# Performance work log

Hardware: AMD Instinct MI355X
Metric: run time of the kernel (lower is better)

## Reference

```python
import jax, jax.numpy as jnp
import numpy as np

HEADS = 16
HEAD_DIM = 64

def setup_inputs() -> dict:
    key = jax.random.key(0)
    ks = jax.random.split(key, 5)
    S, B, H = 1024, 4, 1024
    scale = 1.0 / np.sqrt(H)
    return {
        "hidden_states": jax.random.normal(ks[0], (S, B, H), jnp.float32),
        "attention_mask": jnp.zeros((B * HEADS, 1, S), jnp.float32),
        "Wq": jax.random.normal(ks[1], (H, H), jnp.float32) * scale,
        "bq": jnp.zeros((H,), jnp.float32),
        "Wk": jax.random.normal(ks[2], (H, H), jnp.float32) * scale,
        "bk": jnp.zeros((H,), jnp.float32),
        "Wv": jax.random.normal(ks[3], (H, H), jnp.float32) * scale,
        "bv": jnp.zeros((H,), jnp.float32),
    }

def reference(hidden_states, attention_mask, Wq, bq, Wk, bk, Wv, bv):
    S, B, H = hidden_states.shape
    d = HEAD_DIM
    inv_sqrt_d = 1.0 / np.sqrt(d)
    # QKV projections (torch Linear: x @ W.T + b)
    q = hidden_states @ Wq.T + bq  # (S, B, H)
    k = hidden_states @ Wk.T + bk
    v = hidden_states @ Wv.T + bv
    # (S, B*heads, d) -> (B*heads, S, d)
    q = q.reshape(S, B * HEADS, d).transpose(1, 0, 2)
    k = k.reshape(S, B * HEADS, d).transpose(1, 0, 2)
    v = v.reshape(S, B * HEADS, d).transpose(1, 0, 2)
    # SDDMM: scaled scores + additive mask -> (B*heads, S, S)
    scores = jnp.einsum('nsd,ntd->nst', q, k) * inv_sqrt_d + attention_mask
    probs = jax.nn.softmax(scores, axis=-1)
    # AV bmm -> (B*heads, S, d); note: dropout in source is seeded but never applied
    ctx = jnp.einsum('nst,ntd->nsd', probs, v)
    # back to (S, B, hidden)
    ctx = ctx.transpose(1, 0, 2).reshape(S, B, H)
    return ctx
```

## Files before the change

kernel.cpp:

```cpp
#include <hip/hip_runtime.h>
#include <hip/hip_bf16.h>
#include <math.h>

#define S_LEN 1024
#define BATCH 4
#define HID 1024
#define NHEADS 16
#define DHEAD 64
#define NTOT 64
#define M_ROWS 4096

typedef unsigned short u16;
typedef unsigned int u32;
typedef __bf16 bf16x8 __attribute__((ext_vector_type(8)));
typedef float f32x4 __attribute__((ext_vector_type(4)));

__device__ __forceinline__ u16 f2bf(float x) {
    __hip_bfloat16 h = __float2bfloat16(x);
    return *(u16*)&h;
}

__device__ __forceinline__ void gll16(const u16* g, u16* l) {
    __builtin_amdgcn_global_load_lds(
        (const __attribute__((address_space(1))) u32*)g,
        (__attribute__((address_space(3))) u32*)l, 16, 0, 0);
}

__global__ __launch_bounds__(256) void cvt_all(
    const float* __restrict__ X, const float* __restrict__ wq,
    const float* __restrict__ wk, const float* __restrict__ wv,
    u16* __restrict__ Xb, u16* __restrict__ Wb)
{
    const int bid = blockIdx.x;
    const float* src;
    u16* dst;
    size_t off;
    if (bid < 4096) {
        src = X; dst = Xb; off = (size_t)bid * 1024;
    } else {
        const int wb = bid - 4096;
        const int which = wb >> 10;
        src = (which == 0) ? wq : (which == 1) ? wk : wv;
        dst = Wb + (size_t)which * HID * HID;
        off = (size_t)(wb & 1023) * 1024;
    }
    const size_t idx = off + threadIdx.x * 4;
    float4 x = *(const float4*)(src + idx);
    *(ushort4*)(dst + idx) = make_ushort4(f2bf(x.x), f2bf(x.y), f2bf(x.z), f2bf(x.w));
}

__global__ __launch_bounds__(256, 3) void qkv_mfma(
    const u16* __restrict__ Xb, const u16* __restrict__ Wb,
    const float* __restrict__ bq, const float* __restrict__ bk,
    const float* __restrict__ bv,
    u16* __restrict__ Qb, u16* __restrict__ Kb, u16* __restrict__ VT)
{
    const int m0 = blockIdx.x * 128;
    const int n0 = blockIdx.y * 128;
    const int which = blockIdx.z;

    __shared__ __align__(16) u16 As[128 * 32];
    __shared__ __align__(16) u16 Bs[128 * 32];

    const int tid = threadIdx.x;
    const int lane = tid & 63;
    const int w = tid >> 6;
    const int wm = w & 1, wn = w >> 1;
    const int quad = lane >> 4;
    const int l15 = lane & 15;

    const u16* W = Wb + (size_t)which * HID * HID;

    f32x4 acc[4][4];
    #pragma unroll
    for (int i = 0; i < 4; ++i)
        #pragma unroll
        for (int j = 0; j < 4; ++j)
            #pragma unroll
            for (int r = 0; r < 4; ++r) acc[i][j][r] = 0.0f;

    const int lrow = lane >> 2, lchk = (lane & 3) * 8;

    for (int k0 = 0; k0 < HID; k0 += 32) {
        #pragma unroll
        for (int c = 0; c < 2; ++c) {
            const int seg = w * 2 + c;
            const int row = seg * 16 + lrow;
            gll16(Xb + (size_t)(m0 + row) * HID + k0 + lchk, As + seg * 512);
            gll16(W  + (size_t)(n0 + row) * HID + k0 + lchk, Bs + seg * 512);
        }
        __syncthreads();

        bf16x8 af[4], bf[4];
        #pragma unroll
        for (int i = 0; i < 4; ++i)
            af[i] = *(const bf16x8*)(As + (wm * 64 + i * 16 + l15) * 32 + quad * 8);
        #pragma unroll
        for (int j = 0; j < 4; ++j)
            bf[j] = *(const bf16x8*)(Bs + (wn * 64 + j * 16 + l15) * 32 + quad * 8);
        #pragma unroll
        for (int i = 0; i < 4; ++i)
            #pragma unroll
            for (int j = 0; j < 4; ++j)
                acc[i][j] = __builtin_amdgcn_mfma_f32_16x16x32_bf16(
                    af[i], bf[j], acc[i][j], 0, 0, 0);
        __syncthreads();
    }

    const float* bias = (which == 0) ? bq : (which == 1) ? bk : bv;
    #pragma unroll
    for (int j = 0; j < 4; ++j) {
        const int o = n0 + wn * 64 + j * 16 + l15;
        const float bias_v = bias[o];
        const int head = o >> 6, d = o & 63;
        #pragma unroll
        for (int i = 0; i < 4; ++i) {
            const int mbase = m0 + wm * 64 + i * 16 + quad * 4;
            const int s = mbase >> 2;
            #pragma unroll
            for (int r = 0; r < 4; ++r) {
                const int n = r * NHEADS + head;
                const u16 hv = f2bf(acc[i][j][r] + bias_v);
                if (which == 0)
                    Qb[((size_t)n * S_LEN + s) * DHEAD + d] = hv;
                else if (which == 1)
                    Kb[((size_t)n * S_LEN + s) * DHEAD + d] = hv;
                else
                    VT[(size_t)n * (DHEAD * S_LEN) + (size_t)d * S_LEN + s] = hv;
            }
        }
    }
}

__global__ __launch_bounds__(256, 2) void attn_mfma(
    const u16* __restrict__ Qb, const u16* __restrict__ Kb,
    const u16* __restrict__ VT, const float* __restrict__ mask,
    float* __restrict__ out)
{
    const int n = blockIdx.y;
    const int s0 = blockIdx.x * 128;
    const int b = n >> 4, head = n & 15;

    __shared__ __align__(16) char smem[51200];
    u16* Kbuf = (u16*)smem;
    u16* Vbuf = (u16*)(smem + 16384);
    u16* Ps   = (u16*)(smem + 32768);
    float* Of = (float*)smem;

    const int tid = threadIdx.x;
    const int lane = tid & 63;
    const int w = tid >> 6;
    const int quad = lane >> 4;
    const int l15 = lane & 15;
    const size_t nbase = (size_t)n * S_LEN * DHEAD;

    const int xs0 = ((quad ^ (l15 & 7)) * 8);
    const int xs1 = (((4 + quad) ^ (l15 & 7)) * 8);

    const int srow = lane >> 3;
    const int scg  = (lane & 7) ^ (srow & 7);

    bf16x8 qf[2][2];
    #pragma unroll
    for (int mi = 0; mi < 2; ++mi)
        #pragma unroll
        for (int st = 0; st < 2; ++st)
            qf[mi][st] = *(const bf16x8*)(Qb + nbase +
                (size_t)(s0 + w * 32 + mi * 16 + l15) * 64 + st * 32 + quad * 8);

    f32x4 O[2][4];
    float l_lane[2];
    #pragma unroll
    for (int mi = 0; mi < 2; ++mi) {
        l_lane[mi] = 0.0f;
        #pragma unroll
        for (int jt = 0; jt < 4; ++jt)
            #pragma unroll
            for (int r = 0; r < 4; ++r) O[mi][jt][r] = 0.0f;
    }

    {
        #pragma unroll
        for (int c = 0; c < 2; ++c) {
            const int seg = w * 2 + c;
            const int row = seg * 8 + srow;
            gll16(Kb + nbase + (size_t)row * 64 + scg * 8, Kbuf + seg * 512);
            gll16(VT + nbase + (size_t)row * S_LEN + scg * 8, Vbuf + seg * 512);
        }
    }
    __syncthreads();

    for (int it = 0; it < 16; ++it) {
        const int t0 = it * 64;
        const u16* kb = Kbuf + (it & 1) * 4096;
        const u16* vb = Vbuf + (it & 1) * 4096;

        if (it < 15) {
            u16* kd = Kbuf + ((it + 1) & 1) * 4096;
            u16* vd = Vbuf + ((it + 1) & 1) * 4096;
            #pragma unroll
            for (int c = 0; c < 2; ++c) {
                const int seg = w * 2 + c;
                const int row = seg * 8 + srow;
                gll16(Kb + nbase + (size_t)(t0 + 64 + row) * 64 + scg * 8, kd + seg * 512);
                gll16(VT + nbase + (size_t)row * S_LEN + t0 + 64 + scg * 8, vd + seg * 512);
            }
        }

        f32x4 sc[2][4];
        #pragma unroll
        for (int mi = 0; mi < 2; ++mi)
            #pragma unroll
            for (int j = 0; j < 4; ++j)
                #pragma unroll
                for (int r = 0; r < 4; ++r) sc[mi][j][r] = 0.0f;

        #pragma unroll
        for (int st = 0; st < 2; ++st) {
            const int xo = st ? xs1 : xs0;
            bf16x8 kf[4];
            #pragma unroll
            for (int j = 0; j < 4; ++j)
                kf[j] = *(const bf16x8*)(kb + (j * 16 + l15) * 64 + xo);
            #pragma unroll
            for (int mi = 0; mi < 2; ++mi)
                #pragma unroll
                for (int j = 0; j < 4; ++j)
                    sc[mi][j] = __builtin_amdgcn_mfma_f32_16x16x32_bf16(
                        kf[j], qf[mi][st], sc[mi][j], 0, 0, 0);
        }

        float4 mv4[4];
        #pragma unroll
        for (int j = 0; j < 4; ++j)
            mv4[j] = *(const float4*)(mask + (size_t)n * S_LEN + t0 + j * 16 + quad * 4);

        #pragma unroll
        for (int mi = 0; mi < 2; ++mi) {
            const int q = w * 32 + mi * 16 + l15;
            #pragma unroll
            for (int j = 0; j < 4; ++j) {
                const float p0 = __expf(fmaf(sc[mi][j][0], 0.125f, mv4[j].x - 16.0f));
                const float p1 = __expf(fmaf(sc[mi][j][1], 0.125f, mv4[j].y - 16.0f));
                const float p2 = __expf(fmaf(sc[mi][j][2], 0.125f, mv4[j].z - 16.0f));
                const float p3 = __expf(fmaf(sc[mi][j][3], 0.125f, mv4[j].w - 16.0f));
                l_lane[mi] += (p0 + p1) + (p2 + p3);
                *(ushort4*)(Ps + q * 72 + j * 16 + quad * 4) =
                    make_ushort4(f2bf(p0), f2bf(p1), f2bf(p2), f2bf(p3));
            }
        }

        #pragma unroll
        for (int st = 0; st < 2; ++st) {
            const int xo = st ? xs1 : xs0;
            bf16x8 vf[4];
            #pragma unroll
            for (int jt = 0; jt < 4; ++jt)
                vf[jt] = *(const bf16x8*)(vb + (jt * 16 + l15) * 64 + xo);
            #pragma unroll
            for (int mi = 0; mi < 2; ++mi) {
                bf16x8 pf = *(const bf16x8*)(Ps + (w * 32 + mi * 16 + l15) * 72 +
                                             st * 32 + quad * 8);
                #pragma unroll
                for (int jt = 0; jt < 4; ++jt)
                    O[mi][jt] = __builtin_amdgcn_mfma_f32_16x16x32_bf16(
                        vf[jt], pf, O[mi][jt], 0, 0, 0);
            }
        }

        __syncthreads();
    }

    float inv_l[2];
    #pragma unroll
    for (int mi = 0; mi < 2; ++mi) {
        float l = l_lane[mi];
        l += __shfl_xor(l, 16);
        l += __shfl_xor(l, 32);
        inv_l[mi] = 1.0f / l;
    }
    __syncthreads();

    #pragma unroll
    for (int mi = 0; mi < 2; ++mi) {
        const int q = w * 32 + mi * 16 + l15;
        #pragma unroll
        for (int jt = 0; jt < 4; ++jt)
            #pragma unroll
            for (int r = 0; r < 4; ++r)
                Of[q * 72 + jt * 16 + quad * 4 + r] = O[mi][jt][r] * inv_l[mi];
    }
    __syncthreads();

    const int tx = tid & 15, ty = tid >> 4;
    #pragma unroll
    for (int p = 0; p < 8; ++p) {
        const int q = p * 16 + ty;
        float4 v = *(const float4*)(Of + q * 72 + tx * 4);
        *(float4*)(out + (size_t)(s0 + q) * (BATCH * HID) + (size_t)b * HID +
                   head * DHEAD + tx * 4) = v;
    }
}

extern "C" void kernel_launch(void* const* d_in, const int* in_sizes, int n_in,
                              void* d_out, int out_size, void* d_ws, size_t ws_size,
                              hipStream_t stream)
{
    const float* X    = (const float*)d_in[0];
    const float* mask = (const float*)d_in[1];
    const float* Wq   = (const float*)d_in[2];
    const float* bq   = (const float*)d_in[3];
    const float* Wk   = (const float*)d_in[4];
    const float* bk   = (const float*)d_in[5];
    const float* Wv   = (const float*)d_in[6];
    const float* bv   = (const float*)d_in[7];
    float* out = (float*)d_out;

    const size_t MX = (size_t)M_ROWS * HID;
    const size_t MW = (size_t)HID * HID;
    u16* wsp = (u16*)d_ws;
    u16* Xb = wsp;
    u16* Wb = Xb + MX;
    u16* Qb = Wb + 3 * MW;
    u16* Kb = Qb + MX;
    u16* VT = Kb + MX;

    cvt_all<<<dim3(4096 + 3072), 256, 0, stream>>>(X, Wq, Wk, Wv, Xb, Wb);
    qkv_mfma<<<dim3(M_ROWS / 128, HID / 128, 3), 256, 0, stream>>>(
        Xb, Wb, bq, bk, bv, Qb, Kb, VT);
    attn_mfma<<<dim3(S_LEN / 128, NTOT), 256, 0, stream>>>(Qb, Kb, VT, mask, out);
}
```

Measured before the change: 158.9 us.

## Load K and V fragments directly from global memory, drop LDS double buffer

The attention kernel no longer stages K and V tiles in LDS with async global-to-LDS double buffering. Each wave now reads its MFMA fragments straight from global memory and relies on cache reuse. This removes the per-iteration barrier and shrinks shared memory, so the launch bound rises to 4 blocks per SM for higher occupancy. The risk is redundant global and cache traffic, since every wave re-reads the same K/V data, and load latency that is no longer prefetched. The output write also becomes vectorized float4 stores.

```diff
diff --git a/kernel.cpp b/kernel.cpp
--- a/kernel.cpp
+++ b/kernel.cpp
@@ -132,7 +132,7 @@
     }
 }
 
-__global__ __launch_bounds__(256, 2) void attn_mfma(
+__global__ __launch_bounds__(256, 4) void attn_mfma(
     const u16* __restrict__ Qb, const u16* __restrict__ Kb,
     const u16* __restrict__ VT, const float* __restrict__ mask,
     float* __restrict__ out)
@@ -141,11 +141,9 @@
     const int s0 = blockIdx.x * 128;
     const int b = n >> 4, head = n & 15;
 
-    __shared__ __align__(16) char smem[51200];
-    u16* Kbuf = (u16*)smem;
-    u16* Vbuf = (u16*)(smem + 16384);
-    u16* Ps   = (u16*)(smem + 32768);
+    __shared__ __align__(16) char smem[128 * 72 * 4];
     float* Of = (float*)smem;
+    u16*   Ps = (u16*)smem;
 
     const int tid = threadIdx.x;
     const int lane = tid & 63;
@@ -154,12 +152,6 @@
     const int l15 = lane & 15;
     const size_t nbase = (size_t)n * S_LEN * DHEAD;
 
-    const int xs0 = ((quad ^ (l15 & 7)) * 8);
-    const int xs1 = (((4 + quad) ^ (l15 & 7)) * 8);
-
-    const int srow = lane >> 3;
-    const int scg  = (lane & 7) ^ (srow & 7);
-
     bf16x8 qf[2][2];
     #pragma unroll
     for (int mi = 0; mi < 2; ++mi)
@@ -179,33 +171,12 @@
             for (int r = 0; r < 4; ++r) O[mi][jt][r] = 0.0f;
     }
 
-    {
-        #pragma unroll
-        for (int c = 0; c < 2; ++c) {
-            const int seg = w * 2 + c;
-            const int row = seg * 8 + srow;
-            gll16(Kb + nbase + (size_t)row * 64 + scg * 8, Kbuf + seg * 512);
-            gll16(VT + nbase + (size_t)row * S_LEN + scg * 8, Vbuf + seg * 512);
-        }
-    }
-    __syncthreads();
+    const u16* Kg = Kb + nbase;
+    const u16* Vg = VT + nbase;
+    const float* mg = mask + (size_t)n * S_LEN;
 
     for (int it = 0; it < 16; ++it) {
         const int t0 = it * 64;
-        const u16* kb = Kbuf + (it & 1) * 4096;
-        const u16* vb = Vbuf + (it & 1) * 4096;
-
-        if (it < 15) {
-            u16* kd = Kbuf + ((it + 1) & 1) * 4096;
-            u16* vd = Vbuf + ((it + 1) & 1) * 4096;
-            #pragma unroll
-            for (int c = 0; c < 2; ++c) {
-                const int seg = w * 2 + c;
-                const int row = seg * 8 + srow;
-                gll16(Kb + nbase + (size_t)(t0 + 64 + row) * 64 + scg * 8, kd + seg * 512);
-                gll16(VT + nbase + (size_t)row * S_LEN + t0 + 64 + scg * 8, vd + seg * 512);
-            }
-        }
 
         f32x4 sc[2][4];
         #pragma unroll
@@ -217,11 +188,11 @@
 
         #pragma unroll
         for (int st = 0; st < 2; ++st) {
-            const int xo = st ? xs1 : xs0;
             bf16x8 kf[4];
             #pragma unroll
             for (int j = 0; j < 4; ++j)
-                kf[j] = *(const bf16x8*)(kb + (j * 16 + l15) * 64 + xo);
+                kf[j] = *(const bf16x8*)(Kg + (size_t)(t0 + j * 16 + l15) * 64 +
+                                         st * 32 + quad * 8);
             #pragma unroll
             for (int mi = 0; mi < 2; ++mi)
                 #pragma unroll
@@ -233,7 +204,7 @@
         float4 mv4[4];
         #pragma unroll
         for (int j = 0; j < 4; ++j)
-            mv4[j] = *(const float4*)(mask + (size_t)n * S_LEN + t0 + j * 16 + quad * 4);
+            mv4[j] = *(const float4*)(mg + t0 + j * 16 + quad * 4);
 
         #pragma unroll
         for (int mi = 0; mi < 2; ++mi) {
@@ -252,11 +223,11 @@
 
         #pragma unroll
         for (int st = 0; st < 2; ++st) {
-            const int xo = st ? xs1 : xs0;
             bf16x8 vf[4];
             #pragma unroll
             for (int jt = 0; jt < 4; ++jt)
-                vf[jt] = *(const bf16x8*)(vb + (jt * 16 + l15) * 64 + xo);
+                vf[jt] = *(const bf16x8*)(Vg + (size_t)(jt * 16 + l15) * S_LEN +
+                                          t0 + st * 32 + quad * 8);
             #pragma unroll
             for (int mi = 0; mi < 2; ++mi) {
                 bf16x8 pf = *(const bf16x8*)(Ps + (w * 32 + mi * 16 + l15) * 72 +
@@ -267,8 +238,6 @@
                         vf[jt], pf, O[mi][jt], 0, 0, 0);
             }
         }
-
-        __syncthreads();
     }
 
     float inv_l[2];
@@ -285,10 +254,12 @@
     for (int mi = 0; mi < 2; ++mi) {
         const int q = w * 32 + mi * 16 + l15;
         #pragma unroll
-        for (int jt = 0; jt < 4; ++jt)
-            #pragma unroll
-            for (int r = 0; r < 4; ++r)
-                Of[q * 72 + jt * 16 + quad * 4 + r] = O[mi][jt][r] * inv_l[mi];
+        for (int jt = 0; jt < 4; ++jt) {
+            f32x4 v = O[mi][jt];
+            float4 o4 = make_float4(v[0] * inv_l[mi], v[1] * inv_l[mi],
+                                    v[2] * inv_l[mi], v[3] * inv_l[mi]);
+            *(float4*)(Of + q * 72 + jt * 16 + quad * 4) = o4;
+        }
     }
     __syncthreads();
 
```

Measured after the change: 195.7 us. 1.23x slower.
